# Kernel tuning notes

Measured on AMD Instinct MI355X. Metric: run time of the kernel, lower is better.

The kernel has to match this reference:

```python
import jax, jax.numpy as jnp
import numpy as np

N = 128          # agentNum
S = 128          # stateDim
H = 128          # hiddenSize
IN = S + 4       # per-pair MLP input: state ++ [i, j, a_i, a_j]
P = N * (N - 1) // 2  # number of unordered pairs (each with its own weights)


def setup_inputs() -> dict:
    key = jax.random.key(0)
    ks = jax.random.split(key, 8)
    u = lambda k, shape, fan: jax.random.uniform(
        k, shape, jnp.float32, -1.0 / np.sqrt(fan), 1.0 / np.sqrt(fan))
    return {
        "state":   jax.random.normal(ks[0], (S,), jnp.float32),
        "actions": jax.random.normal(ks[1], (N,), jnp.float32),
        "W1": u(ks[2], (P, IN, H), IN),
        "b1": u(ks[3], (P, H), IN),
        "W2": u(ks[4], (P, H, H), H),
        "b2": u(ks[5], (P, H), H),
        "W3": u(ks[6], (P, H, 2), H),
        "b3": u(ks[7], (P, 2), H),
    }


def reference(state, actions, W1, b1, W2, b2, W3, b3):
    n = actions.shape[0]
    ii_np, jj_np = np.triu_indices(n, 1)      # static pair index lists, i < j
    ii = jnp.asarray(ii_np)
    jj = jnp.asarray(jj_np)
    p = ii.shape[0]
    dt = state.dtype
    # per-pair input: [state, i, j, actions[i], actions[j]] -> [P, S+4]
    x = jnp.concatenate([
        jnp.broadcast_to(state, (p, state.shape[0])),
        ii[:, None].astype(dt),
        jj[:, None].astype(dt),
        actions[ii][:, None],
        actions[jj][:, None],
    ], axis=1)
    # batched per-pair 3-layer MLP (each pair has its own weights)
    h = jax.nn.relu(jnp.einsum('pi,pih->ph', x, W1) + b1)
    h = jax.nn.relu(jnp.einsum('ph,phk->pk', h, W2) + b2)
    g = jax.nn.softmax(jnp.einsum('ph,pho->po', h, W3) + b3, axis=-1)  # [P, 2]
    # lambda_[a] = sum over all pairs containing agent a (scatter-sum on both endpoints)
    lam = jnp.zeros((n, 2), g.dtype).at[ii].add(g).at[jj].add(g)
    return lam
```

## Files before the change

kernel.cpp:

```cpp
#include <hip/hip_runtime.h>

#define N_AG    128
#define H_DIM   128
#define IN_DIM  132
#define P_PAIRS 8128
#define BLOCKS  1016

typedef float f32x4 __attribute__((ext_vector_type(4)));

__device__ __forceinline__ void pair_from_p(int p, int& i, int& j) {
    int t = P_PAIRS - 1 - p;
    float kf = (sqrtf(8.f * (float)t + 1.f) - 1.f) * 0.5f;
    int k = (int)kf;
    while ((k + 1) * (k + 2) / 2 <= t) ++k;
    while (k * (k + 1) / 2 > t) --k;
    i = N_AG - 2 - k;
    j = N_AG - 1 - (t - k * (k + 1) / 2);
}

__global__ void zero_out_kernel(float* out) { out[threadIdx.x] = 0.f; }

__global__ __launch_bounds__(256, 4) void fused_mlp_kernel(
    const float* __restrict__ state,
    const float* __restrict__ actions,
    const float* __restrict__ W1,
    const float* __restrict__ b1,
    const float* __restrict__ W2,
    const float* __restrict__ b2,
    const float* __restrict__ W3,
    const float* __restrict__ b3,
    float* __restrict__ out)
{
    const int t    = threadIdx.x;
    const int slot = t >> 5;
    const int lane = t & 31;
    const int p    = blockIdx.x * 8 + slot;

    __shared__ float xss[8][128];
    __shared__ float h1s[8][128];

    #pragma unroll
    for (int q = 0; q < 4; ++q)
        xss[slot][lane + 32 * q] = state[lane + 32 * q];

    int i, j;
    pair_from_p(p, i, j);
    const float x128 = (float)i;
    const float x129 = (float)j;
    const float x130 = actions[i];
    const float x131 = actions[j];

    __builtin_amdgcn_wave_barrier();

    const f32x4* W1p = (const f32x4*)(W1 + (size_t)p * (IN_DIM * H_DIM));
    f32x4 acc = (f32x4)(0.f);
    #pragma unroll 8
    for (int r = 0; r < 128; ++r) {
        const float xv = xss[slot][r];
        const f32x4 w = __builtin_nontemporal_load(&W1p[r * 32 + lane]);
        acc.x = fmaf(xv, w.x, acc.x);
        acc.y = fmaf(xv, w.y, acc.y);
        acc.z = fmaf(xv, w.z, acc.z);
        acc.w = fmaf(xv, w.w, acc.w);
    }
    {
        const f32x4 wA = __builtin_nontemporal_load(&W1p[128 * 32 + lane]);
        const f32x4 wB = __builtin_nontemporal_load(&W1p[129 * 32 + lane]);
        const f32x4 wC = __builtin_nontemporal_load(&W1p[130 * 32 + lane]);
        const f32x4 wD = __builtin_nontemporal_load(&W1p[131 * 32 + lane]);
        acc.x = fmaf(x128, wA.x, acc.x); acc.y = fmaf(x128, wA.y, acc.y);
        acc.z = fmaf(x128, wA.z, acc.z); acc.w = fmaf(x128, wA.w, acc.w);
        acc.x = fmaf(x129, wB.x, acc.x); acc.y = fmaf(x129, wB.y, acc.y);
        acc.z = fmaf(x129, wB.z, acc.z); acc.w = fmaf(x129, wB.w, acc.w);
        acc.x = fmaf(x130, wC.x, acc.x); acc.y = fmaf(x130, wC.y, acc.y);
        acc.z = fmaf(x130, wC.z, acc.z); acc.w = fmaf(x130, wC.w, acc.w);
        acc.x = fmaf(x131, wD.x, acc.x); acc.y = fmaf(x131, wD.y, acc.y);
        acc.z = fmaf(x131, wD.z, acc.z); acc.w = fmaf(x131, wD.w, acc.w);
    }
    const f32x4 b1v = *(const f32x4*)(b1 + (size_t)p * H_DIM + 4 * lane);
    f32x4 h1;
    h1.x = fmaxf(acc.x + b1v.x, 0.f);
    h1.y = fmaxf(acc.y + b1v.y, 0.f);
    h1.z = fmaxf(acc.z + b1v.z, 0.f);
    h1.w = fmaxf(acc.w + b1v.w, 0.f);
    *(f32x4*)&h1s[slot][4 * lane] = h1;

    __builtin_amdgcn_wave_barrier();

    const f32x4* W2p = (const f32x4*)(W2 + (size_t)p * (H_DIM * H_DIM));
    acc = (f32x4)(0.f);
    #pragma unroll 8
    for (int k = 0; k < 128; ++k) {
        const float hv = h1s[slot][k];
        const f32x4 w = __builtin_nontemporal_load(&W2p[k * 32 + lane]);
        acc.x = fmaf(hv, w.x, acc.x);
        acc.y = fmaf(hv, w.y, acc.y);
        acc.z = fmaf(hv, w.z, acc.z);
        acc.w = fmaf(hv, w.w, acc.w);
    }
    const f32x4 b2v = *(const f32x4*)(b2 + (size_t)p * H_DIM + 4 * lane);
    f32x4 h2;
    h2.x = fmaxf(acc.x + b2v.x, 0.f);
    h2.y = fmaxf(acc.y + b2v.y, 0.f);
    h2.z = fmaxf(acc.z + b2v.z, 0.f);
    h2.w = fmaxf(acc.w + b2v.w, 0.f);

    const f32x4* W3p = (const f32x4*)(W3 + (size_t)p * (H_DIM * 2));
    const f32x4 wa = __builtin_nontemporal_load(&W3p[2 * lane]);
    const f32x4 wb = __builtin_nontemporal_load(&W3p[2 * lane + 1]);
    float l0 = h2.x * wa.x + h2.y * wa.z + h2.z * wb.x + h2.w * wb.z;
    float l1 = h2.x * wa.y + h2.y * wa.w + h2.z * wb.y + h2.w * wb.w;
    #pragma unroll
    for (int off = 16; off > 0; off >>= 1) {
        l0 += __shfl_xor(l0, off, 32);
        l1 += __shfl_xor(l1, off, 32);
    }
    if (lane == 0) {
        l0 += b3[2 * p];
        l1 += b3[2 * p + 1];
        const float m  = fmaxf(l0, l1);
        const float e0 = expf(l0 - m), e1 = expf(l1 - m);
        const float inv = 1.f / (e0 + e1);
        const float g0 = e0 * inv, g1 = e1 * inv;
        atomicAdd(&out[2 * i],     g0);
        atomicAdd(&out[2 * i + 1], g1);
        atomicAdd(&out[2 * j],     g0);
        atomicAdd(&out[2 * j + 1], g1);
    }
}

extern "C" void kernel_launch(void* const* d_in, const int* in_sizes, int n_in,
                              void* d_out, int out_size, void* d_ws, size_t ws_size,
                              hipStream_t stream) {
    const float* state   = (const float*)d_in[0];
    const float* actions = (const float*)d_in[1];
    const float* W1      = (const float*)d_in[2];
    const float* b1      = (const float*)d_in[3];
    const float* W2      = (const float*)d_in[4];
    const float* b2      = (const float*)d_in[5];
    const float* W3      = (const float*)d_in[6];
    const float* b3      = (const float*)d_in[7];
    float* out = (float*)d_out;

    zero_out_kernel<<<1, 256, 0, stream>>>(out);
    fused_mlp_kernel<<<BLOCKS, 256, 0, stream>>>(
        state, actions, W1, b1, W2, b2, W3, b3, out);
}
```

Before: 203.1 us.

## Use full 64-lane wavefront per pair with split-K and shuffle reduction

Each pair is now processed by a full 64-lane wavefront instead of 32 threads. The two half-waves each handle alternate input rows and combine partial sums with a cross-half shuffle. Blocks drop to 4 pairs, the grid doubles, and launch bounds ask for higher occupancy. The goal is to use whole wavefronts for memory loads on this bandwidth-bound weight stream, at the cost of extra shuffles, an extra LDS buffer and idle half-waves during the bias/ReLU steps.

```diff
diff --git a/kernel.cpp b/kernel.cpp
--- a/kernel.cpp
+++ b/kernel.cpp
@@ -4,7 +4,8 @@
 #define H_DIM   128
 #define IN_DIM  132
 #define P_PAIRS 8128
-#define BLOCKS  1016
+#define PPB     4
+#define BLOCKS  2032
 
 typedef float f32x4 __attribute__((ext_vector_type(4)));
 
@@ -20,7 +21,7 @@
 
 __global__ void zero_out_kernel(float* out) { out[threadIdx.x] = 0.f; }
 
-__global__ __launch_bounds__(256, 4) void fused_mlp_kernel(
+__global__ __launch_bounds__(256, 8) void fused_mlp_kernel(
     const float* __restrict__ state,
     const float* __restrict__ actions,
     const float* __restrict__ W1,
@@ -32,16 +33,18 @@
     float* __restrict__ out)
 {
     const int t    = threadIdx.x;
-    const int slot = t >> 5;
-    const int lane = t & 31;
-    const int p    = blockIdx.x * 8 + slot;
+    const int slot = __builtin_amdgcn_readfirstlane(t >> 6);
+    const int lane = t & 63;
+    const int h    = lane >> 5;
+    const int c    = lane & 31;
+    const int p    = blockIdx.x * PPB + slot;
 
-    __shared__ float xss[8][128];
-    __shared__ float h1s[8][128];
+    __shared__ float xss[PPB][128];
+    __shared__ float h1s[PPB][128];
+    __shared__ float h2s[PPB][128];
 
-    #pragma unroll
-    for (int q = 0; q < 4; ++q)
-        xss[slot][lane + 32 * q] = state[lane + 32 * q];
+    xss[slot][lane]      = state[lane];
+    xss[slot][lane + 64] = state[lane + 64];
 
     int i, j;
     pair_from_p(p, i, j);
@@ -54,66 +57,76 @@
 
     const f32x4* W1p = (const f32x4*)(W1 + (size_t)p * (IN_DIM * H_DIM));
     f32x4 acc = (f32x4)(0.f);
-    #pragma unroll 8
-    for (int r = 0; r < 128; ++r) {
-        const float xv = xss[slot][r];
-        const f32x4 w = __builtin_nontemporal_load(&W1p[r * 32 + lane]);
+    #pragma unroll 4
+    for (int k = 0; k < 64; ++k) {
+        const float xv = xss[slot][2 * k + h];
+        const f32x4 w = __builtin_nontemporal_load(&W1p[k * 64 + lane]);
         acc.x = fmaf(xv, w.x, acc.x);
         acc.y = fmaf(xv, w.y, acc.y);
         acc.z = fmaf(xv, w.z, acc.z);
         acc.w = fmaf(xv, w.w, acc.w);
     }
     {
-        const f32x4 wA = __builtin_nontemporal_load(&W1p[128 * 32 + lane]);
-        const f32x4 wB = __builtin_nontemporal_load(&W1p[129 * 32 + lane]);
-        const f32x4 wC = __builtin_nontemporal_load(&W1p[130 * 32 + lane]);
-        const f32x4 wD = __builtin_nontemporal_load(&W1p[131 * 32 + lane]);
-        acc.x = fmaf(x128, wA.x, acc.x); acc.y = fmaf(x128, wA.y, acc.y);
-        acc.z = fmaf(x128, wA.z, acc.z); acc.w = fmaf(x128, wA.w, acc.w);
-        acc.x = fmaf(x129, wB.x, acc.x); acc.y = fmaf(x129, wB.y, acc.y);
-        acc.z = fmaf(x129, wB.z, acc.z); acc.w = fmaf(x129, wB.w, acc.w);
-        acc.x = fmaf(x130, wC.x, acc.x); acc.y = fmaf(x130, wC.y, acc.y);
-        acc.z = fmaf(x130, wC.z, acc.z); acc.w = fmaf(x130, wC.w, acc.w);
-        acc.x = fmaf(x131, wD.x, acc.x); acc.y = fmaf(x131, wD.y, acc.y);
-        acc.z = fmaf(x131, wD.z, acc.z); acc.w = fmaf(x131, wD.w, acc.w);
+        const f32x4 wA = __builtin_nontemporal_load(&W1p[64 * 64 + lane]);
+        const float xa = h ? x129 : x128;
+        acc.x = fmaf(xa, wA.x, acc.x); acc.y = fmaf(xa, wA.y, acc.y);
+        acc.z = fmaf(xa, wA.z, acc.z); acc.w = fmaf(xa, wA.w, acc.w);
+        const f32x4 wB = __builtin_nontemporal_load(&W1p[65 * 64 + lane]);
+        const float xb = h ? x131 : x130;
+        acc.x = fmaf(xb, wB.x, acc.x); acc.y = fmaf(xb, wB.y, acc.y);
+        acc.z = fmaf(xb, wB.z, acc.z); acc.w = fmaf(xb, wB.w, acc.w);
     }
-    const f32x4 b1v = *(const f32x4*)(b1 + (size_t)p * H_DIM + 4 * lane);
-    f32x4 h1;
-    h1.x = fmaxf(acc.x + b1v.x, 0.f);
-    h1.y = fmaxf(acc.y + b1v.y, 0.f);
-    h1.z = fmaxf(acc.z + b1v.z, 0.f);
-    h1.w = fmaxf(acc.w + b1v.w, 0.f);
-    *(f32x4*)&h1s[slot][4 * lane] = h1;
-
+    acc.x += __shfl_xor(acc.x, 32, 64);
+    acc.y += __shfl_xor(acc.y, 32, 64);
+    acc.z += __shfl_xor(acc.z, 32, 64);
+    acc.w += __shfl_xor(acc.w, 32, 64);
+    const f32x4 b1v = *(const f32x4*)(b1 + (size_t)p * H_DIM + 4 * c);
+    if (h == 0) {
+        f32x4 h1v;
+        h1v.x = fmaxf(acc.x + b1v.x, 0.f);
+        h1v.y = fmaxf(acc.y + b1v.y, 0.f);
+        h1v.z = fmaxf(acc.z + b1v.z, 0.f);
+        h1v.w = fmaxf(acc.w + b1v.w, 0.f);
+        *(f32x4*)&h1s[slot][4 * c] = h1v;
+    }
     __builtin_amdgcn_wave_barrier();
 
     const f32x4* W2p = (const f32x4*)(W2 + (size_t)p * (H_DIM * H_DIM));
     acc = (f32x4)(0.f);
-    #pragma unroll 8
-    for (int k = 0; k < 128; ++k) {
-        const float hv = h1s[slot][k];
-        const f32x4 w = __builtin_nontemporal_load(&W2p[k * 32 + lane]);
+    #pragma unroll 4
+    for (int k = 0; k < 64; ++k) {
+        const float hv = h1s[slot][2 * k + h];
+        const f32x4 w = __builtin_nontemporal_load(&W2p[k * 64 + lane]);
         acc.x = fmaf(hv, w.x, acc.x);
         acc.y = fmaf(hv, w.y, acc.y);
         acc.z = fmaf(hv, w.z, acc.z);
         acc.w = fmaf(hv, w.w, acc.w);
     }
-    const f32x4 b2v = *(const f32x4*)(b2 + (size_t)p * H_DIM + 4 * lane);
-    f32x4 h2;
-    h2.x = fmaxf(acc.x + b2v.x, 0.f);
-    h2.y = fmaxf(acc.y + b2v.y, 0.f);
-    h2.z = fmaxf(acc.z + b2v.z, 0.f);
-    h2.w = fmaxf(acc.w + b2v.w, 0.f);
+    acc.x += __shfl_xor(acc.x, 32, 64);
+    acc.y += __shfl_xor(acc.y, 32, 64);
+    acc.z += __shfl_xor(acc.z, 32, 64);
+    acc.w += __shfl_xor(acc.w, 32, 64);
+    const f32x4 b2v = *(const f32x4*)(b2 + (size_t)p * H_DIM + 4 * c);
+    if (h == 0) {
+        f32x4 h2v;
+        h2v.x = fmaxf(acc.x + b2v.x, 0.f);
+        h2v.y = fmaxf(acc.y + b2v.y, 0.f);
+        h2v.z = fmaxf(acc.z + b2v.z, 0.f);
+        h2v.w = fmaxf(acc.w + b2v.w, 0.f);
+        *(f32x4*)&h2s[slot][4 * c] = h2v;
+    }
+    __builtin_amdgcn_wave_barrier();
 
     const f32x4* W3p = (const f32x4*)(W3 + (size_t)p * (H_DIM * 2));
-    const f32x4 wa = __builtin_nontemporal_load(&W3p[2 * lane]);
-    const f32x4 wb = __builtin_nontemporal_load(&W3p[2 * lane + 1]);
-    float l0 = h2.x * wa.x + h2.y * wa.z + h2.z * wb.x + h2.w * wb.z;
-    float l1 = h2.x * wa.y + h2.y * wa.w + h2.z * wb.y + h2.w * wb.w;
+    const f32x4 w3 = __builtin_nontemporal_load(&W3p[lane]);
+    const float h2a = h2s[slot][2 * lane];
+    const float h2b = h2s[slot][2 * lane + 1];
+    float l0 = h2a * w3.x + h2b * w3.z;
+    float l1 = h2a * w3.y + h2b * w3.w;
     #pragma unroll
-    for (int off = 16; off > 0; off >>= 1) {
-        l0 += __shfl_xor(l0, off, 32);
-        l1 += __shfl_xor(l1, off, 32);
+    for (int off = 32; off > 0; off >>= 1) {
+        l0 += __shfl_xor(l0, off, 64);
+        l1 += __shfl_xor(l1, off, 64);
     }
     if (lane == 0) {
         l0 += b3[2 * p];
```

New measurement: 203.6 us. Within noise of the previous version (+0.2%).
